# Kernel tuning notes

Measured on AMD Instinct MI355X. Metric: run time of the kernel, lower is better.

Reference implementation:

```python
import jax, jax.numpy as jnp
import numpy as np

N = 30000; E = 480000; B = 60
IN = 200; ID = 128; H = 128
NEXP = 4; TOPK = 2; TEMP = 1.5
HEADS = 4; DH = H // HEADS


def _ln(x, g, b):
    mu = jnp.mean(x, -1, keepdims=True)
    var = jnp.var(x, -1, keepdims=True)
    return (x - mu) / jnp.sqrt(var + 1e-5) * g + b


def _seg_sum(d, i, n):
    return jax.ops.segment_sum(d, i, num_segments=n)


def setup_inputs():
    key = jax.random.key(0)
    kit = iter(jax.random.split(key, 80))
    def w(*s):
        return jax.random.normal(next(kit), s, jnp.float32) * 0.05
    inp = {}
    inp['x'] = jax.random.normal(next(kit), (N, IN), jnp.float32)
    inp['node_identity'] = jax.random.normal(next(kit), (N, ID), jnp.float32)
    inp['edge_index'] = jax.random.randint(next(kit), (2, E), 0, N)
    inp['batch'] = jnp.sort(jax.random.randint(next(kit), (N,), 0, B))
    inp.update(fe_W=w(IN, H), fe_b=jnp.zeros(H), fe_g=jnp.ones(H), fe_be=jnp.zeros(H))
    inp.update(ie_W=w(ID, H), ie_b=jnp.zeros(H), ie_g=jnp.ones(H), ie_be=jnp.zeros(H))
    inp.update(fuse_W=w(2 * H, H), fuse_b=jnp.zeros(H), fuse_g=jnp.ones(H), fuse_be=jnp.zeros(H))
    inp.update(router_W=w(2 * H, NEXP))
    inp.update(mlp_W1=w(H, H), mlp_b1=jnp.zeros(H), mlp_W2=w(H, H), mlp_b2=jnp.zeros(H))
    inp.update(cheb_W=w(2, 2, H, H), cheb_b=jnp.zeros((2, H)))
    inp.update(gt_Wq=w(2, H, H), gt_bq=jnp.zeros((2, H)), gt_Wk=w(2, H, H), gt_bk=jnp.zeros((2, H)),
               gt_Wv=w(2, H, H), gt_bv=jnp.zeros((2, H)), gt_Ws=w(2, H, H), gt_bs=jnp.zeros((2, H)))
    inp.update(gcn_W=w(2, H, H), gcn_b=jnp.zeros((2, H)))
    inp.update(pn_g=jnp.ones((NEXP, H)), pn_b=jnp.zeros((NEXP, H)), expert_scales=jnp.ones(NEXP))
    inp.update(h1_W=w(H, H), h1_b=jnp.zeros(H), h1_g=jnp.ones(H), h1_be=jnp.zeros(H))
    inp.update(h2_W=w(H, H // 2), h2_b=jnp.zeros(H // 2), h2_g=jnp.ones(H // 2), h2_be=jnp.zeros(H // 2))
    inp.update(h3_W=w(H // 2, 2), h3_b=jnp.zeros(2), logit_bias=jnp.zeros(2))
    return inp


def _forward(x, node_identity, edge_index, batch, fe_W, fe_b, fe_g, fe_be, ie_W, ie_b, ie_g, ie_be,
             fuse_W, fuse_b, fuse_g, fuse_be, router_W, mlp_W1, mlp_b1, mlp_W2, mlp_b2, cheb_W, cheb_b,
             gt_Wq, gt_bq, gt_Wk, gt_bk, gt_Wv, gt_bv, gt_Ws, gt_bs, gcn_W, gcn_b, pn_g, pn_b,
             expert_scales, h1_W, h1_b, h1_g, h1_be, h2_W, h2_b, h2_g, h2_be, h3_W, h3_b, logit_bias):
    relu = jax.nn.relu
    src, dst = edge_index[0], edge_index[1]
    # encoders + fuse
    h_x = relu(_ln(x @ fe_W + fe_b, fe_g, fe_be))
    h_id = relu(_ln(node_identity @ ie_W + ie_b, ie_g, ie_be))
    h_router = jnp.concatenate([h_x, h_id], -1)
    h = relu(_ln(h_router @ fuse_W + fuse_b, fuse_g, fuse_be))
    # noisy top-k router (eval: no noise, no dropout)
    node_logits = h_router @ router_W
    probs = jax.nn.softmax(node_logits / TEMP, -1)
    vals, idx = jax.lax.top_k(probs, TOPK)
    wts = vals / jnp.clip(jnp.sum(vals, -1, keepdims=True), 1e-9)
    gates = jnp.zeros_like(probs).at[jnp.arange(N)[:, None], idx].set(wts)  # [N, 4]
    # degree / normalization terms
    ones_e = jnp.ones(E, jnp.float32)
    deg = _seg_sum(ones_e, dst, N)
    dinv = jnp.where(deg > 0, jax.lax.rsqrt(jnp.maximum(deg, 1.0)), 0.0)
    dinvl = jax.lax.rsqrt(deg + 1.0)  # with self loops (GCN)
    enorm = dinv[src] * dinv[dst]
    enorml = dinvl[src] * dinvl[dst]
    def aprop(xx, en, di_self=None):
        out = _seg_sum(xx[src] * en[:, None], dst, N)
        if di_self is not None:
            out = out + xx * di_self[:, None]
        return out
    # Expert 0: MLP (2 layers)
    e0 = relu(h @ mlp_W1 + mlp_b1) @ mlp_W2 + mlp_b2
    # Expert 1: ChebNet K=2 (lambda_max=2 -> L_hat = -A_norm), 2 layers
    z = h
    for l in range(2):
        tx1 = -aprop(z, enorm)
        z = z @ cheb_W[l, 0] + tx1 @ cheb_W[l, 1] + cheb_b[l]
        if l == 0:
            z = relu(z)
    e1 = z
    # Expert 2: Graph Transformer, 2 layers, heads=4, root-weight skip
    z = h
    for l in range(2):
        q = (z @ gt_Wq[l] + gt_bq[l]).reshape(N, HEADS, DH)
        k = (z @ gt_Wk[l] + gt_bk[l]).reshape(N, HEADS, DH)
        v = (z @ gt_Wv[l] + gt_bv[l]).reshape(N, HEADS, DH)
        logits = jnp.sum(q[dst] * k[src], -1) * (1.0 / DH ** 0.5)  # [E, heads]
        m = jax.ops.segment_max(logits, dst, num_segments=N)
        m = jnp.where(jnp.isfinite(m), m, 0.0)
        p = jnp.exp(logits - m[dst])
        denom = jnp.clip(_seg_sum(p, dst, N), 1e-9)
        attn = p / denom[dst]
        agg = _seg_sum(attn[:, :, None] * v[src], dst, N).reshape(N, H)
        z = agg + z @ gt_Ws[l] + gt_bs[l]
        if l == 0:
            z = relu(z)
    e2 = z
    # Expert 3: GCN, 2 layers, self loops
    z = h
    for l in range(2):
        zw = z @ gcn_W[l]
        z = aprop(zw, enorml, dinvl * dinvl) + gcn_b[l]
        if l == 0:
            z = relu(z)
    e3 = z
    # per-expert post-norm, scale, gated combine + residual
    eo = jnp.stack([e0, e1, e2, e3], 0)  # [4, N, H]
    eo = _ln(eo, pn_g[:, None, :], pn_b[:, None, :]) * expert_scales[:, None, None]
    out = h + jnp.einsum('ne,enh->nh', gates, eo)
    # mean-pool readout per graph
    counts = jnp.clip(_seg_sum(jnp.ones(N, jnp.float32), batch, B), 1.0)
    pooled = _seg_sum(out, batch, B) / counts[:, None]
    # classification head
    zc = relu(_ln(pooled @ h1_W + h1_b, h1_g, h1_be))
    zc = relu(_ln(zc @ h2_W + h2_b, h2_g, h2_be))
    return zc @ h3_W + h3_b + logit_bias


def reference(x, node_identity, edge_index, batch, fe_W, fe_b, fe_g, fe_be, ie_W, ie_b, ie_g, ie_be,
              fuse_W, fuse_b, fuse_g, fuse_be, router_W, mlp_W1, mlp_b1, mlp_W2, mlp_b2, cheb_W, cheb_b,
              gt_Wq, gt_bq, gt_Wk, gt_bk, gt_Wv, gt_bv, gt_Ws, gt_bs, gcn_W, gcn_b, pn_g, pn_b,
              expert_scales, h1_W, h1_b, h1_g, h1_be, h2_W, h2_b, h2_g, h2_be, h3_W, h3_b, logit_bias):
    return _forward(x, node_identity, edge_index, batch, fe_W, fe_b, fe_g, fe_be, ie_W, ie_b, ie_g, ie_be,
                    fuse_W, fuse_b, fuse_g, fuse_be, router_W, mlp_W1, mlp_b1, mlp_W2, mlp_b2, cheb_W, cheb_b,
                    gt_Wq, gt_bq, gt_Wk, gt_bk, gt_Wv, gt_bv, gt_Ws, gt_bs, gcn_W, gcn_b, pn_g, pn_b,
                    expert_scales, h1_W, h1_b, h1_g, h1_be, h2_W, h2_b, h2_g, h2_be, h3_W, h3_b, logit_bias)
```

## Files before the change

kernel.cpp:

```cpp
#include <hip/hip_runtime.h>

#define PCH   32
#define NWT   19
#define SCH   2048

typedef unsigned short ushort_t;
typedef __attribute__((ext_vector_type(8))) short bf16x8;
typedef __attribute__((ext_vector_type(4))) float f32x4;

__device__ __forceinline__ float bf2f(unsigned int v) {
    return __uint_as_float(v << 16);
}
__device__ __forceinline__ unsigned int f2bu(float f) {
    unsigned int u = __float_as_uint(f);
    return (u + 0x7fffu + ((u >> 16) & 1u)) >> 16;
}
__device__ __forceinline__ void unpack8(uint4 u, float* f) {
    f[0] = bf2f(u.x & 0xffff); f[1] = bf2f(u.x >> 16);
    f[2] = bf2f(u.y & 0xffff); f[3] = bf2f(u.y >> 16);
    f[4] = bf2f(u.z & 0xffff); f[5] = bf2f(u.z >> 16);
    f[6] = bf2f(u.w & 0xffff); f[7] = bf2f(u.w >> 16);
}
__device__ __forceinline__ uint4 pack8(const float* f) {
    uint4 p;
// ... 596 lines not shown
            *(uint4*)&Bs[rows[j]][kofs[j] + 8] = bvb[j][1];
        }
        __syncthreads();
#pragma unroll
        for (int t = 16; t < 32; t++) {
            bf16x8 bf = *(const bf16x8*)&Bs[(t - 16) * 16 + l16][q * 8];
            acc[t] = __builtin_amdgcn_mfma_f32_16x16x32_bf16(af, bf, acc[t], 0, 0, 0);
        }
    }
    const float* bs4[4] = {b0, b1, b2, b3};
#pragma unroll
    for (int s = 0; s < 4; s++) {
#pragma unroll
        for (int t8 = 0; t8 < 8; t8++) {
            int t = s * 8 + t8;
            int col = t8 * 16 + l16;
            float bb = bs4[s][col];
#pragma unroll
            for (int r = 0; r < 4; r++) {
                int row = m0 + 16 * wv + q * 4 + r;
                float val = acc[t][r] + bb;
                float other = __shfl_xor(val, 1);
                if (!(lane & 1) && row < M) {
                    unsigned int pk = f2bu(val) | (f2bu(other) << 16);
                    if (s == 0)
                        *(unsigned int*)(qb + (size_t)row * 128 + col) = pk;
                    else if (s == 3)
                        *(unsigned int*)(sk + (size_t)row * 128 + col) = pk;
                    else
                        *(unsigned int*)(kv + (size_t)row * 256 + (s - 1) * 128 + col) = pk;
                }
            }
        }
    }
}

__device__ __forceinline__ void gemm_wv_dev(const ushort_t* __restrict__ A,
                                            const ushort_t* __restrict__ Wt,
                                            ushort_t* __restrict__ Cb, int M,
                                            const float* __restrict__ bias, int relu,
                                            int w, int lane)
{
    const int K = 128;
    int ct = w & 3;
    int rt = w >> 2;
    int row0 = rt * 16;
    if (row0 >= M) return;
    int l16 = lane & 15, q = lane >> 4;
    int arow = row0 + l16;
    bool aok = arow < M;
    const ushort_t* Ar = A + (size_t)arow * K + q * 8;
    const ushort_t* W0 = Wt + (size_t)(ct * 32 + l16) * K + q * 8;
    const ushort_t* W1 = W0 + (size_t)16 * K;
    bf16x8 zz = {0, 0, 0, 0, 0, 0, 0, 0};
    f32x4 a0 = {0.f, 0.f, 0.f, 0.f}, a1 = {0.f, 0.f, 0.f, 0.f};
#pragma unroll
    for (int k0 = 0; k0 < K; k0 += 32) {
        bf16x8 af = aok ? *(const bf16x8*)(Ar + k0) : zz;
        bf16x8 b0 = *(const bf16x8*)(W0 + k0);
        bf16x8 b1 = *(const bf16x8*)(W1 + k0);
        a0 = __builtin_amdgcn_mfma_f32_16x16x32_bf16(af, b0, a0, 0, 0, 0);
        a1 = __builtin_amdgcn_mfma_f32_16x16x32_bf16(af, b1, a1, 0, 0, 0);
    }
    f32x4 av[2] = {a0, a1};
#pragma unroll
    for (int t = 0; t < 2; t++) {
        int col = ct * 32 + t * 16 + l16;
        float bb = bias ? bias[col] : 0.f;
#pragma unroll
        for (int r = 0; r < 4; r++) {
            int row = row0 + q * 4 + r;
            float val = av[t][r] + bb;
            if (relu) val = fmaxf(val, 0.f);
            float other = __shfl_xor(val, 1);
            if (!(l16 & 1) && row < M) {
                unsigned int pk = f2bu(val) | (f2bu(other) << 16);
                *(unsigned int*)(Cb + (size_t)row * 128 + col) = pk;
            }
        }
    }
}

__device__ __forceinline__ void gather2_dev(const ushort_t* __restrict__ Xb,
                                            ushort_t* __restrict__ OutA, ushort_t* __restrict__ OutB,
                                            const int* __restrict__ rowptr, const int* __restrict__ csr,
                                            const float* __restrict__ ecA, const float* __restrict__ ecB,
                                            const float* __restrict__ dinvl, int M, int bx)
{
    int node = bx * 4 + (threadIdx.x >> 6);
    int lane = threadIdx.x & 63;
    if (node >= M) return;
    int beg = rowptr[node], end = rowptr[node + 1];
    int slot = lane >> 4, g = lane & 15;
    float aA[8] = {0, 0, 0, 0, 0, 0, 0, 0};
    float aB[8] = {0, 0, 0, 0, 0, 0, 0, 0};

    float cAa = 0.f, cBa = 0.f, cAb = 0.f, cBb = 0.f;
    int na = 0, nb = 0;
    float nAa = 0.f, nBa = 0.f, nAb = 0.f, nBb = 0.f;
    uint4 xA, xB;
    {
        int r0 = beg + slot, r1 = beg + 4 + slot;
        int ia = 0, ib = 0;
        if (r0 < end) { ia = csr[r0]; cAa = ecA[r0]; cBa = ecB[r0]; }
        if (r1 < end) { ib = csr[r1]; cAb = ecA[r1]; cBb = ecB[r1]; }
        xA = *(const uint4*)(Xb + (size_t)ia * 128 + g * 8);
        xB = *(const uint4*)(Xb + (size_t)ib * 128 + g * 8);
    }
    {
        int r0 = beg + 8 + slot, r1 = beg + 12 + slot;
        if (r0 < end) { na = csr[r0]; nAa = ecA[r0]; nBa = ecB[r0]; }
        if (r1 < end) { nb = csr[r1]; nAb = ecA[r1]; nBb = ecB[r1]; }
    }
    for (int e = beg; e < end; e += 8) {
        uint4 xA2 = *(const uint4*)(Xb + (size_t)na * 128 + g * 8);
        uint4 xB2 = *(const uint4*)(Xb + (size_t)nb * 128 + g * 8);
        int r0 = e + 16 + slot, r1 = e + 20 + slot;
        int ma = 0, mb = 0;
        float mAa = 0.f, mBa = 0.f, mAb = 0.f, mBb = 0.f;
        if (r0 < end) { ma = csr[r0]; mAa = ecA[r0]; mBa = ecB[r0]; }
        if (r1 < end) { mb = csr[r1]; mAb = ecA[r1]; mBb = ecB[r1]; }
        fma8(xA, cAa, aA); fma8(xA, cBa, aB);
        fma8(xB, cAb, aA); fma8(xB, cBb, aB);
        xA = xA2; xB = xB2;
        cAa = nAa; cBa = nBa; cAb = nAb; cBb = nBb;
        na = ma; nb = mb;
        nAa = mAa; nBa = mBa; nAb = mAb; nBb = mBb;
    }
#pragma unroll
    for (int j = 0; j < 8; j++) {
        aA[j] += __shfl_xor(aA[j], 16); aA[j] += __shfl_xor(aA[j], 32);
        aB[j] += __shfl_xor(aB[j], 16); aB[j] += __shfl_xor(aB[j], 32);
    }
    {
        float c = dinvl[node]; c *= c;
        uint4 xs = *(const uint4*)(Xb + (size_t)node * 128 + g * 8);
        fma8(xs, c, aB);
    }
    if (lane < 16) {
        float oA[8], oB[8];
#pragma unroll
        for (int j = 0; j < 8; j++) { oA[j] = -aA[j]; oB[j] = aB[j]; }
        size_t ofs = (size_t)node * 128 + g * 8;
        *(uint4*)(OutA + ofs) = pack8(oA);
        *(uint4*)(OutB + ofs) = pack8(oB);
    }
}

__device__ __forceinline__ void gather_l2_dev(const ushort_t* __restrict__ XA,
                                              const ushort_t* __restrict__ XB,
                                              ushort_t* __restrict__ OutA, ushort_t* __restrict__ OutB,
                                              const int* __restrict__ rowptr, const int* __restrict__ csr,
                                              const float* __restrict__ ecA, const float* __restrict__ ecB,
                                              const float* __restrict__ dinvl, int M, int bx)
{
    int node = bx * 4 + (threadIdx.x >> 6);
    int lane = threadIdx.x & 63;
    if (node >= M) return;
    int beg = rowptr[node], end = rowptr[node + 1];
    int slot = lane >> 4, g = lane & 15;
    float aA[8] = {0, 0, 0, 0, 0, 0, 0, 0};
    float aB[8] = {0, 0, 0, 0, 0, 0, 0, 0};

    float cAa = 0.f, cBa = 0.f, cAb = 0.f, cBb = 0.f;
    int na = 0, nb = 0;
    float nAa = 0.f, nBa = 0.f, nAb = 0.f, nBb = 0.f;
    uint4 ra, rb, sa, sb;
    {
        int r0 = beg + slot, r1 = beg + 4 + slot;
        int ia = 0, ib = 0;
        if (r0 < end) { ia = csr[r0]; cAa = ecA[r0]; cBa = ecB[r0]; }
        if (r1 < end) { ib = csr[r1]; cAb = ecA[r1]; cBb = ecB[r1]; }
        ra = *(const uint4*)(XA + (size_t)ia * 128 + g * 8);
        rb = *(const uint4*)(XA + (size_t)ib * 128 + g * 8);
        sa = *(const uint4*)(XB + (size_t)ia * 128 + g * 8);
        sb = *(const uint4*)(XB + (size_t)ib * 128 + g * 8);
    }
    {
        int r0 = beg + 8 + slot, r1 = beg + 12 + slot;
        if (r0 < end) { na = csr[r0]; nAa = ecA[r0]; nBa = ecB[r0]; }
        if (r1 < end) { nb = csr[r1]; nAb = ecA[r1]; nBb = ecB[r1]; }
    }
    for (int e = beg; e < end; e += 8) {
        uint4 ra2 = *(const uint4*)(XA + (size_t)na * 128 + g * 8);
        uint4 rb2 = *(const uint4*)(XA + (size_t)nb * 128 + g * 8);
        uint4 sa2 = *(const uint4*)(XB + (size_t)na * 128 + g * 8);
        uint4 sb2 = *(const uint4*)(XB + (size_t)nb * 128 + g * 8);
        int r0 = e + 16 + slot, r1 = e + 20 + slot;
        int ma = 0, mb = 0;
        float mAa = 0.f, mBa = 0.f, mAb = 0.f, mBb = 0.f;
        if (r0 < end) { ma = csr[r0]; mAa = ecA[r0]; mBa = ecB[r0]; }
        if (r1 < end) { mb = csr[r1]; mAb = ecA[r1]; mBb = ecB[r1]; }
        fma8(ra, cAa, aA); fma8(rb, cAb, aA);
        fma8(sa, cBa, aB); fma8(sb, cBb, aB);
        ra = ra2; rb = rb2; sa = sa2; sb = sb2;
        cAa = nAa; cBa = nBa; cAb = nAb; cBb = nBb;
        na = ma; nb = mb;
        nAa = mAa; nBa = mBa; nAb = mAb; nBb = mBb;
    }
#pragma unroll
    for (int j = 0; j < 8; j++) {
        aA[j] += __shfl_xor(aA[j], 16); aA[j] += __shfl_xor(aA[j], 32);
        aB[j] += __shfl_xor(aB[j], 16); aB[j] += __shfl_xor(aB[j], 32);
    }
    {
        float c = dinvl[node]; c *= c;
        uint4 xs = *(const uint4*)(XB + (size_t)node * 128 + g * 8);
        fma8(xs, c, aB);
    }
    if (lane < 16) {
        float oA[8], oB[8];
#pragma unroll
        for (int j = 0; j < 8; j++) { oA[j] = -aA[j]; oB[j] = aB[j]; }
        size_t ofs = (size_t)node * 128 + g * 8;
        *(uint4*)(OutA + ofs) = pack8(oA);
        *(uint4*)(OutB + ofs) = pack8(oB);
    }
}

__device__ __forceinline__ void gt_attn_dev(const ushort_t* __restrict__ Qb,
                                            const ushort_t* __restrict__ KV,
                                            const int* __restrict__ rowptr, const int* __restrict__ csr,
                                            const ushort_t* __restrict__ sk, int relu,
                                            ushort_t* __restrict__ Outb, int M, int bx)
{
    const float SCL = 0.17677669529663689f * 1.4426950408889634f;
    int node = bx * 4 + (threadIdx.x >> 6);
    int lane = threadIdx.x & 63;
    if (node >= M) return;
    int beg = rowptr[node], end = rowptr[node + 1];
    int slot = lane >> 4, g = lane & 15;
    uint4 qv = *(const uint4*)(Qb + (size_t)node * 128 + g * 8);
    float qf[8];
    unpack8(qv, qf);
#pragma unroll
    for (int j = 0; j < 8; j++) qf[j] *= SCL;
    float ax[8] = {0, 0, 0, 0, 0, 0, 0, 0};
    float den = 0.f;

    bool va = false, vb = false;
    int na = 0, nb = 0;
    bool wa = false, wb = false;
    uint4 kA, kB, uA, uB;
    {
        int r0 = beg + slot, r1 = beg + 4 + slot;
        va = r0 < end; vb = r1 < end;
        int ia = va ? csr[r0] : 0;
        int ib = vb ? csr[r1] : 0;
        const ushort_t* p0 = KV + (size_t)ia * 256 + g * 8;
        const ushort_t* p1 = KV + (size_t)ib * 256 + g * 8;
        kA = *(const uint4*)p0; uA = *(const uint4*)(p0 + 128);
        kB = *(const uint4*)p1; uB = *(const uint4*)(p1 + 128);
    }
    {
        int r0 = beg + 8 + slot, r1 = beg + 12 + slot;
        wa = r0 < end; wb = r1 < end;
        na = wa ? csr[r0] : 0;
        nb = wb ? csr[r1] : 0;
    }
    for (int e = beg; e < end; e += 8) {
        const ushort_t* p0 = KV + (size_t)na * 256 + g * 8;
        const ushort_t* p1 = KV + (size_t)nb * 256 + g * 8;
        uint4 kA2 = *(const uint4*)p0;
        uint4 uA2 = *(const uint4*)(p0 + 128);
        uint4 kB2 = *(const uint4*)p1;
        uint4 uB2 = *(const uint4*)(p1 + 128);
        int r0 = e + 16 + slot, r1 = e + 20 + slot;
        bool xa = r0 < end, xb = r1 < end;
        int ma = xa ? csr[r0] : 0;
        int mb = xb ? csr[r1] : 0;
        float d0 = dot8(kA, qf);
        float d1 = dot8(kB, qf);
        d0 += __shfl_xor(d0, 1); d0 += __shfl_xor(d0, 2);
        d1 += __shfl_xor(d1, 1); d1 += __shfl_xor(d1, 2);
        float w0 = va ? exp2f(fminf(d0, 80.f)) : 0.f;
        float w1 = vb ? exp2f(fminf(d1, 80.f)) : 0.f;
        den += w0 + w1;
        fma8(uA, w0, ax);
        fma8(uB, w1, ax);
        kA = kA2; kB = kB2; uA = uA2; uB = uB2;
        va = wa; vb = wb;
        wa = xa; wb = xb; na = ma; nb = mb;
    }
#pragma unroll
    for (int j = 0; j < 8; j++) {
        ax[j] += __shfl_xor(ax[j], 16); ax[j] += __shfl_xor(ax[j], 32);
    }
    den += __shfl_xor(den, 16); den += __shfl_xor(den, 32);
    float dd = fmaxf(den, 1e-9f);
    if (lane < 16) {
        uint4 sv = *(const uint4*)(sk + (size_t)node * 128 + g * 8);
        float sf[8];
        unpack8(sv, sf);
        float o[8];
#pragma unroll
        for (int j = 0; j < 8; j++) {
            float v = ax[j] / dd + sf[j];
            o[j] = relu ? fmaxf(v, 0.f) : v;
        }
        *(uint4*)(Outb + (size_t)node * 128 + g * 8) = pack8(o);
    }
}

__global__ void flatA_kernel(const ushort_t* __restrict__ hb,
                             ushort_t* __restrict__ x1, ushort_t* __restrict__ x2,
                             const int* __restrict__ rowptr, const int* __restrict__ csr,
                             const float* __restrict__ ecA, const float* __restrict__ ecB,
                             const float* __restrict__ dinvl, int N,
                             const ushort_t* __restrict__ wmlp1, ushort_t* __restrict__ xm,
                             const float* __restrict__ b18)
{
    int bx = blockIdx.x;
    int gN4 = (N + 3) >> 2;
    if (bx < gN4) {
        gather2_dev(hb, x1, x2, rowptr, csr, ecA, ecB, dinvl, N, bx);
    } else {
        int w = (bx - gN4) * 4 + (threadIdx.x >> 6);
        gemm_wv_dev(hb, wmlp1, xm, N, b18, 1, w, threadIdx.x & 63);
    }
}

__global__ __launch_bounds__(256)
void megaA_kernel(const ushort_t* __restrict__ hb,
                  const ushort_t* __restrict__ wqkvs,
                  ushort_t* __restrict__ qb, ushort_t* __restrict__ kvb, ushort_t* __restrict__ skb,
                  const float* __restrict__ bq, const float* __restrict__ bk,
                  const float* __restrict__ bv, const float* __restrict__ bs,
                  const ushort_t* __restrict__ x1, const ushort_t* __restrict__ wch0,
                  const ushort_t* __restrict__ wch1, ushort_t* __restrict__ x0,
                  const float* __restrict__ bch,
                  const ushort_t* __restrict__ x2, const ushort_t* __restrict__ wgcn,
                  ushort_t* __restrict__ xg1, const float* __restrict__ bgcn,
                  int M)
{
    __shared__ ushort_t As[64][40];
    __shared__ ushort_t Bs[256][40];
    int y = blockIdx.y, bx = blockIdx.x;
    if (y == 0) gemm4_dev(As, Bs, hb, wqkvs, qb, kvb, skb, M, bq, bk, bv, bs, bx);
    else if (y == 1) gemm_dual_dev(As, Bs, hb, wch0, x1, wch1, x0, M, bch, 1, bx);
    else gemm_bf_dev<128>(As, Bs, x2, wgcn, xg1, M, bgcn, 1, bx);
}

__global__ void flatB_kernel(const ushort_t* __restrict__ qb, const ushort_t* __restrict__ kvb,
                             const int* __restrict__ rowptr, const int* __restrict__ csr,
                             const ushort_t* __restrict__ skb, ushort_t* __restrict__ aout,
                             const ushort_t* __restrict__ x0, const ushort_t* __restrict__ xg1,
                             ushort_t* __restrict__ x3, ushort_t* __restrict__ x2,
                             const float* __restrict__ ecA, const float* __restrict__ ecB,
                             const float* __restrict__ dinvl, int N)
{
    int bx = blockIdx.x;
    int gN4 = (N + 3) >> 2;
    if (bx < gN4) gt_attn_dev(qb, kvb, rowptr, csr, skb, 1, aout, N, bx);
    else gather_l2_dev(x0, xg1, x3, x2, rowptr, csr, ecA, ecB, dinvl, N, bx - gN4);
}

__global__ __launch_bounds__(256)
void megaB_kernel(const ushort_t* __restrict__ x1,
                  const ushort_t* __restrict__ wqkvs,
                  ushort_t* __restrict__ qb, ushort_t* __restrict__ kvb, ushort_t* __restrict__ skb,
                  const float* __restrict__ bq, const float* __restrict__ bk,
                  const float* __restrict__ bv, const float* __restrict__ bs,
                  const ushort_t* __restrict__ x0, const ushort_t* __restrict__ wch0,
                  const ushort_t* __restrict__ x3, const ushort_t* __restrict__ wch1,
                  ushort_t* __restrict__ e1b, const float* __restrict__ bch,
                  const ushort_t* __restrict__ x2, const ushort_t* __restrict__ wgcn,
                  ushort_t* __restrict__ e3b, const float* __restrict__ bgcn,
                  const ushort_t* __restrict__ xm, const ushort_t* __restrict__ wmlp2,
                  ushort_t* __restrict__ e0b, const float* __restrict__ bmlp2,
                  int M)
{
    __shared__ ushort_t As[64][40];
    __shared__ ushort_t Bs[256][40];
    int y = blockIdx.y, bx = blockIdx.x;
    if (y == 0) gemm4_dev(As, Bs, x1, wqkvs, qb, kvb, skb, M, bq, bk, bv, bs, bx);
    else if (y == 1) gemm_dual_dev(As, Bs, x0, wch0, x3, wch1, e1b, M, bch, 0, bx);
    else if (y == 2) gemm_bf_dev<128>(As, Bs, x2, wgcn, e3b, M, bgcn, 0, bx);
    else gemm_bf_dev<128>(As, Bs, xm, wmlp2, e0b, M, bmlp2, 0, bx);
}

__global__ void gt_attn2_kernel(const ushort_t* __restrict__ Qb, const ushort_t* __restrict__ KV,
                                const int* __restrict__ rowptr, const int* __restrict__ csr,
                                const ushort_t* __restrict__ sk,
                                ushort_t* __restrict__ Outb, int M)
{
    gt_attn_dev(Qb, KV, rowptr, csr, sk, 0, Outb, M, blockIdx.x);
}

__global__ void pool_combine_kernel(const ushort_t* __restrict__ hb,
                                    const ushort_t* __restrict__ e0, const ushort_t* __restrict__ e1,
                                    const ushort_t* __restrict__ e2, const ushort_t* __restrict__ e3,
                                    const float* __restrict__ gates,
                                    const float* __restrict__ png, const float* __restrict__ pnb,
                                    const float* __restrict__ esc,
                                    const int* __restrict__ bstart, const int* __restrict__ bend,
                                    float* __restrict__ partial)
{
    int b = blockIdx.x, c = blockIdx.y;
    int lane = threadIdx.x;
    int s0 = bstart[b], e0i = bend[b];
    const ushort_t* eps[4] = {e0, e1, e2, e3};
    float ga[4], gb[4], ba[4], bb[4], es[4];
#pragma unroll
    for (int ee = 0; ee < 4; ee++) {
        ga[ee] = png[ee * 128 + lane * 2];
        gb[ee] = png[ee * 128 + lane * 2 + 1];
        ba[ee] = pnb[ee * 128 + lane * 2];
        bb[ee] = pnb[ee * 128 + lane * 2 + 1];
        es[ee] = esc[ee];
    }
    float sx = 0.f, sy = 0.f;
    for (int n = s0 + c; n < e0i; n += PCH) {
        size_t ofs = (size_t)n * 128 + lane * 2;
        float4 gg = *(const float4*)(gates + (size_t)n * 4);
        float gv[4] = {gg.x, gg.y, gg.z, gg.w};
        unsigned int hu = *(const unsigned int*)(hb + ofs);
        float ox = bf2f(hu & 0xffff), oy = bf2f(hu >> 16);
#pragma unroll
        for (int ee = 0; ee < 4; ee++) {
            unsigned int u = *(const unsigned int*)(eps[ee] + ofs);
            float vx = bf2f(u & 0xffff), vy = bf2f(u >> 16);
            float su = vx + vy, sq = vx * vx + vy * vy;
#pragma unroll
            for (int off = 32; off; off >>= 1) { su += __shfl_xor(su, off); sq += __shfl_xor(sq, off); }
            float mean = su * (1.f / 128.f);
            float var = sq * (1.f / 128.f) - mean * mean;
            float inv = rsqrtf(var + 1e-5f);
            float cc = es[ee] * gv[ee];
            ox = fmaf(cc, (vx - mean) * inv * ga[ee] + ba[ee], ox);
            oy = fmaf(cc, (vy - mean) * inv * gb[ee] + bb[ee], oy);
        }
        sx += ox; sy += oy;
    }
    *(float2*)(partial + ((size_t)b * PCH + c) * 128 + lane * 2) = make_float2(sx, sy);
}

__global__ void head_kernel(const float* __restrict__ partial,
                            const int* __restrict__ bstart, const int* __restrict__ bend,
                            const float* __restrict__ h1W, const float* __restrict__ h1b,
                            const float* __restrict__ h1g, const float* __restrict__ h1be,
                            const float* __restrict__ h2W, const float* __restrict__ h2b,
                            const float* __restrict__ h2g, const float* __restrict__ h2be,
                            const float* __restrict__ h3W, const float* __restrict__ h3b,
                            const float* __restrict__ lbias,
                            float* __restrict__ out, int B)
{
    __shared__ float p[128], z[128];
    int b = blockIdx.x, t = threadIdx.x;
    float sum = 0.f;
#pragma unroll
    for (int c = 0; c < PCH; c++) sum += partial[((size_t)b * PCH + c) * 128 + t];
    float cnt = fmaxf((float)(bend[b] - bstart[b]), 1.f);
    p[t] = sum / cnt;
    __syncthreads();
    float a = h1b[t];
    for (int k = 0; k < 128; k++) a = fmaf(p[k], h1W[k * 128 + t], a);
    z[t] = a;
    __syncthreads();
    float s = 0.f, sq = 0.f;
    for (int k = 0; k < 128; k++) { float x = z[k]; s += x; sq += x * x; }
    float mean = s * (1.f / 128.f), var = sq * (1.f / 128.f) - mean * mean;
    float y = fmaxf((a - mean) * rsqrtf(var + 1e-5f) * h1g[t] + h1be[t], 0.f);
    __syncthreads();
    z[t] = y;
    __syncthreads();
    float a2 = 0.f;
    if (t < 64) {
        a2 = h2b[t];
        for (int k = 0; k < 128; k++) a2 = fmaf(z[k], h2W[k * 64 + t], a2);
    }
    __syncthreads();
    if (t < 64) p[t] = a2;
    __syncthreads();
    if (t < 2) {
        float s2 = 0.f, sq2 = 0.f;
        for (int k = 0; k < 64; k++) { float x = p[k]; s2 += x; sq2 += x * x; }
        float mean2 = s2 * (1.f / 64.f), var2 = sq2 * (1.f / 64.f) - mean2 * mean2;
        float inv2 = rsqrtf(var2 + 1e-5f);
        float o = h3b[t] + lbias[t];
        for (int k = 0; k < 64; k++) {
            float zc = fmaxf((p[k] - mean2) * inv2 * h2g[k] + h2be[k], 0.f);
            o = fmaf(zc, h3W[k * 2 + t], o);
        }
        out[b * 2 + t] = o;
    }
}

extern "C" void kernel_launch(void* const* d_in, const int* in_sizes, int n_in,
                              void* d_out, int out_size, void* d_ws, size_t ws_size,
                              hipStream_t stream)
{
    (void)ws_size; (void)n_in;
    const int N = in_sizes[3];
    const int E = in_sizes[2] / 2;
    const int B = out_size / 2;

    const int* ei = (const int*)d_in[2];
    const int* src = ei;
    const int* dst = ei + E;
    const int* batch = (const int*)d_in[3];

    const float* W[47];
    for (int i = 0; i < 47; i++) W[i] = (const float*)d_in[i];

    size_t fN = (size_t)N;
    float* gates   = (float*)d_ws;
    float* dinv    = gates + 4 * fN;
    float* dinvl   = dinv + fN;
    float* partial = dinvl + fN;
    float* logitsA = partial + (size_t)128 * B * PCH;
    float* logitsB = logitsA + 4 * fN;
    ushort_t* hb  = (ushort_t*)(logitsB + 4 * fN);
    ushort_t* e0b = hb + 128 * fN;
    ushort_t* e1b = e0b + 128 * fN;
    ushort_t* e2b = e1b + 128 * fN;
    ushort_t* e3b = e2b + 128 * fN;
    ushort_t* x0  = e3b + 128 * fN;
    ushort_t* x1  = x0 + 128 * fN;
    ushort_t* x2  = x1 + 128 * fN;
    ushort_t* x3  = x2 + 128 * fN;
    ushort_t* xm  = x3 + 128 * fN;
    ushort_t* xg1 = xm + 128 * fN;
    ushort_t* skb = xg1 + 128 * fN;
    ushort_t* qb  = skb + 128 * fN;
    ushort_t* kvb = qb + 128 * fN;
    ushort_t* hrb = kvb + 256 * fN;
    ushort_t* wt  = hrb + 256 * fN;
    WtPack wp;
    const float* wsrc[NWT] = {
        W[4], W[8], W[12], W[17], W[19],
        W[21], W[21] + 16384, W[21] + 32768, W[21] + 49152,
        W[23], W[25], W[27], W[29],
        W[23] + 16384, W[25] + 16384, W[27] + 16384, W[29] + 16384,
        W[31], W[31] + 16384
    };
    const int wk[NWT] = {200, 128, 256, 128, 128,
                         128, 128, 128, 128,
                         128, 128, 128, 128,
                         128, 128, 128, 128,
                         128, 128};
    unsigned long long woff[NWT];
    unsigned long long acc_off = 0;
    for (int i = 0; i < NWT; i++) {
        wp.src[i] = wsrc[i];
        wp.K[i] = wk[i];
        wp.off[i] = acc_off;
        woff[i] = acc_off;
        acc_off += (unsigned long long)128 * wk[i];
    }
    int* degi   = (int*)(wt + acc_off + 8);
    int* cursor = degi + N;
    int* rowptr = cursor + N;
    int* csr    = rowptr + (N + 1);
    int* bstart = csr + E;
    int* bend   = bstart + B;
    int* bsum   = bend + B;
    float* ecA  = (float*)(bsum + 256);
    float* ecB  = ecA + E;

    dim3 blk(256);
    int gN4 = (N + 3) / 4;
    int gG = (N + 63) / 64;
    int RT = (N + 15) / 16;
    int nsb = (N + SCH - 1) / SCH;
    int nseg = (N + 255) / 256;
    int nedge = (E + 255) / 256;

    hipMemsetAsync(degi, 0, (size_t)2 * N * sizeof(int), stream);
    hipMemsetAsync(bstart, 0, (size_t)2 * B * sizeof(int), stream);

    setup_mega_kernel<<<dim3(608 + nseg + nedge), blk, 0, stream>>>(
        wp, wt, batch, bstart, bend, N, dst, degi, E);
    scan1_kernel<<<dim3(nsb), blk, 0, stream>>>(degi, rowptr, bsum, N);
    scan2_kernel<<<1, blk, 0, stream>>>(bsum, nsb);
    EncCfg c0 = {W[0], 200, 200, wt + woff[0], hrb, W[5], W[6], W[7], W[16], logitsA};
    EncCfg c1 = {W[1], 128, 128, wt + woff[1], hrb + 128, W[9], W[10], W[11], W[16] + 512, logitsB};
    scan3_enc_kernel<<<dim3(nseg + 2 * gG), blk, 0, stream>>>(
        rowptr, bsum, degi, dinv, dinvl, N, c0, c1);
    ln_csr_topk_kernel<<<dim3(gG + nedge + nseg), blk, 0, stream>>>(
        hrb, wt + woff[2], hb, N, W[13], W[14], W[15],
        src, dst, rowptr, cursor, csr, dinv, dinvl, ecA, ecB, E,
        logitsA, logitsB, gates);
    flatA_kernel<<<dim3(gN4 + RT), blk, 0, stream>>>(hb, x1, x2, rowptr, csr, ecA, ecB,
                                                     dinvl, N, wt + woff[3], xm, W[18]);
    megaA_kernel<<<dim3(gG, 3), blk, 0, stream>>>(
        hb, wt + woff[9], qb, kvb, skb, W[24], W[26], W[28], W[30],
        x1, wt + woff[5], wt + woff[6], x0, W[22],
        x2, wt + woff[17], xg1, W[32], N);
    flatB_kernel<<<dim3(2 * gN4), blk, 0, stream>>>(
        qb, kvb, rowptr, csr, skb, x1,
        x0, xg1, x3, x2, ecA, ecB, dinvl, N);
    megaB_kernel<<<dim3(gG, 4), blk, 0, stream>>>(
        x1, wt + woff[13], qb, kvb, skb,
        W[24] + 128, W[26] + 128, W[28] + 128, W[30] + 128,
        x0, wt + woff[7], x3, wt + woff[8], e1b, W[22] + 128,
        x2, wt + woff[18], e3b, W[32] + 128,
        xm, wt + woff[4], e0b, W[20], N);
    gt_attn2_kernel<<<dim3(gN4), blk, 0, stream>>>(qb, kvb, rowptr, csr, skb, e2b, N);
    pool_combine_kernel<<<dim3(B, PCH), dim3(64), 0, stream>>>(
        hb, e0b, e1b, e2b, e3b, gates, W[33], W[34], W[35], bstart, bend, partial);
    head_kernel<<<dim3(B), dim3(128), 0, stream>>>(partial, bstart, bend,
        W[36], W[37], W[38], W[39],
        W[40], W[41], W[42], W[43],
        W[44], W[45], W[46],
        (float*)d_out, B);
}
```

Baseline: 546.6 us.

## Regroup expert stages into four launches mixing gathers, attention and GEMMs

Reorders the dependency schedule of the four expert branches. The five launches (flatA, megaA, flatB, megaB, gt_attn2) become four fused stage kernels. Each stage mixes independent memory-bound gather/attention blocks with compute-bound GEMM blocks, and the MLP second layer moves to the wavefront GEMV path. A separate buffer xa1 holds the first attention output so it no longer overwrites x1, and the Chebyshev/GCN stages use a smaller 128-row B tile in shared memory. The aim is to remove one launch and its barrier and to overlap heterogeneous work. The cost is that heterogeneous blocks in one grid compete for occupancy and may be unevenly balanced.

```diff
diff --git a/kernel.cpp b/kernel.cpp
--- a/kernel.cpp
+++ b/kernel.cpp
@@ -922,89 +922,102 @@
     }
 }
 
-__global__ void flatA_kernel(const ushort_t* __restrict__ hb,
-                             ushort_t* __restrict__ x1, ushort_t* __restrict__ x2,
-                             const int* __restrict__ rowptr, const int* __restrict__ csr,
-                             const float* __restrict__ ecA, const float* __restrict__ ecB,
-                             const float* __restrict__ dinvl, int N,
-                             const ushort_t* __restrict__ wmlp1, ushort_t* __restrict__ xm,
-                             const float* __restrict__ b18)
-{
+__global__ __launch_bounds__(256)
+void stage1_kernel(const ushort_t* __restrict__ hb,
+                   ushort_t* __restrict__ x1, ushort_t* __restrict__ x2,
+                   const int* __restrict__ rowptr, const int* __restrict__ csr,
+                   const float* __restrict__ ecA, const float* __restrict__ ecB,
+                   const float* __restrict__ dinvl, int N,
+                   const ushort_t* __restrict__ wmlp1, ushort_t* __restrict__ xm,
+                   const float* __restrict__ bmlp1,
+                   const ushort_t* __restrict__ wqkvs,
+                   ushort_t* __restrict__ qb, ushort_t* __restrict__ kvb,
+                   ushort_t* __restrict__ skb,
+                   const float* __restrict__ bq, const float* __restrict__ bk,
+                   const float* __restrict__ bv, const float* __restrict__ bs)
+{
+    __shared__ ushort_t As[64][40];
+    __shared__ ushort_t Bs[256][40];
     int bx = blockIdx.x;
     int gN4 = (N + 3) >> 2;
+    int RT = (N + 15) >> 4;
     if (bx < gN4) {
         gather2_dev(hb, x1, x2, rowptr, csr, ecA, ecB, dinvl, N, bx);
+    } else if (bx < gN4 + RT) {
+        int w = (bx - gN4) * 4 + (threadIdx.x >> 6);
+        gemm_wv_dev(hb, wmlp1, xm, N, bmlp1, 1, w, threadIdx.x & 63);
     } else {
-        int w = (bx - gN4) * 4 + (threadIdx.x >> 6);
-        gemm_wv_dev(hb, wmlp1, xm, N, b18, 1, w, threadIdx.x & 63);
+        gemm4_dev(As, Bs, hb, wqkvs, qb, kvb, skb, N, bq, bk, bv, bs, bx - gN4 - RT);
     }
 }
 
 __global__ __launch_bounds__(256)
-void megaA_kernel(const ushort_t* __restrict__ hb,
-                  const ushort_t* __restrict__ wqkvs,
-                  ushort_t* __restrict__ qb, ushort_t* __restrict__ kvb, ushort_t* __restrict__ skb,
-                  const float* __restrict__ bq, const float* __restrict__ bk,
-                  const float* __restrict__ bv, const float* __restrict__ bs,
-                  const ushort_t* __restrict__ x1, const ushort_t* __restrict__ wch0,
-                  const ushort_t* __restrict__ wch1, ushort_t* __restrict__ x0,
-                  const float* __restrict__ bch,
-                  const ushort_t* __restrict__ x2, const ushort_t* __restrict__ wgcn,
-                  ushort_t* __restrict__ xg1, const float* __restrict__ bgcn,
-                  int M)
+void stage2_kernel(const ushort_t* __restrict__ qb, const ushort_t* __restrict__ kvb,
+                   const int* __restrict__ rowptr, const int* __restrict__ csr,
+                   const ushort_t* __restrict__ skb, ushort_t* __restrict__ xa1,
+                   const ushort_t* __restrict__ hb, const ushort_t* __restrict__ wch0,
+                   const ushort_t* __restrict__ x1, const ushort_t* __restrict__ wch1,
+                   ushort_t* __restrict__ x0, const float* __restrict__ bch,
+                   const ushort_t* __restrict__ x2, const ushort_t* __restrict__ wgcn,
+                   ushort_t* __restrict__ xg1, const float* __restrict__ bgcn, int N)
+{
+    __shared__ ushort_t As[64][40];
+    __shared__ ushort_t Bs[128][40];
+    int bx = blockIdx.x;
+    int gN4 = (N + 3) >> 2;
+    int gG = (N + 63) >> 6;
+    if (bx < gN4) gt_attn_dev(qb, kvb, rowptr, csr, skb, 1, xa1, N, bx);
+    else if (bx < gN4 + gG) gemm_dual_dev(As, Bs, hb, wch0, x1, wch1, x0, N, bch, 1, bx - gN4);
+    else gemm_bf_dev<128>(As, Bs, x2, wgcn, xg1, N, bgcn, 1, bx - gN4 - gG);
+}
+
+__global__ __launch_bounds__(256)
+void stage3_kernel(const ushort_t* __restrict__ x0, const ushort_t* __restrict__ xg1,
+                   ushort_t* __restrict__ x3, ushort_t* __restrict__ x2,
+                   const int* __restrict__ rowptr, const int* __restrict__ csr,
+                   const float* __restrict__ ecA, const float* __restrict__ ecB,
+                   const float* __restrict__ dinvl, int N,
+                   const ushort_t* __restrict__ xm, const ushort_t* __restrict__ wmlp2,
+                   ushort_t* __restrict__ e0b, const float* __restrict__ bmlp2,
+                   const ushort_t* __restrict__ xa1, const ushort_t* __restrict__ wqkvs,
+                   ushort_t* __restrict__ qb, ushort_t* __restrict__ kvb,
+                   ushort_t* __restrict__ skb,
+                   const float* __restrict__ bq, const float* __restrict__ bk,
+                   const float* __restrict__ bv, const float* __restrict__ bs)
 {
     __shared__ ushort_t As[64][40];
     __shared__ ushort_t Bs[256][40];
-    int y = blockIdx.y, bx = blockIdx.x;
-    if (y == 0) gemm4_dev(As, Bs, hb, wqkvs, qb, kvb, skb, M, bq, bk, bv, bs, bx);
-    else if (y == 1) gemm_dual_dev(As, Bs, hb, wch0, x1, wch1, x0, M, bch, 1, bx);
-    else gemm_bf_dev<128>(As, Bs, x2, wgcn, xg1, M, bgcn, 1, bx);
-}
-
-__global__ void flatB_kernel(const ushort_t* __restrict__ qb, const ushort_t* __restrict__ kvb,
-                             const int* __restrict__ rowptr, const int* __restrict__ csr,
-                             const ushort_t* __restrict__ skb, ushort_t* __restrict__ aout,
-                             const ushort_t* __restrict__ x0, const ushort_t* __restrict__ xg1,
-                             ushort_t* __restrict__ x3, ushort_t* __restrict__ x2,
-                             const float* __restrict__ ecA, const float* __restrict__ ecB,
-                             const float* __restrict__ dinvl, int N)
-{
     int bx = blockIdx.x;
     int gN4 = (N + 3) >> 2;
-    if (bx < gN4) gt_attn_dev(qb, kvb, rowptr, csr, skb, 1, aout, N, bx);
-    else gather_l2_dev(x0, xg1, x3, x2, rowptr, csr, ecA, ecB, dinvl, N, bx - gN4);
+    int RT = (N + 15) >> 4;
+    if (bx < gN4) {
+        gather_l2_dev(x0, xg1, x3, x2, rowptr, csr, ecA, ecB, dinvl, N, bx);
+    } else if (bx < gN4 + RT) {
+        int w = (bx - gN4) * 4 + (threadIdx.x >> 6);
+        gemm_wv_dev(xm, wmlp2, e0b, N, bmlp2, 0, w, threadIdx.x & 63);
+    } else {
+        gemm4_dev(As, Bs, xa1, wqkvs, qb, kvb, skb, N, bq, bk, bv, bs, bx - gN4 - RT);
+    }
 }
 
 __global__ __launch_bounds__(256)
-void megaB_kernel(const ushort_t* __restrict__ x1,
-                  const ushort_t* __restrict__ wqkvs,
-                  ushort_t* __restrict__ qb, ushort_t* __restrict__ kvb, ushort_t* __restrict__ skb,
-                  const float* __restrict__ bq, const float* __restrict__ bk,
-                  const float* __restrict__ bv, const float* __restrict__ bs,
-                  const ushort_t* __restrict__ x0, const ushort_t* __restrict__ wch0,
-                  const ushort_t* __restrict__ x3, const ushort_t* __restrict__ wch1,
-                  ushort_t* __restrict__ e1b, const float* __restrict__ bch,
-                  const ushort_t* __restrict__ x2, const ushort_t* __restrict__ wgcn,
-                  ushort_t* __restrict__ e3b, const float* __restrict__ bgcn,
-                  const ushort_t* __restrict__ xm, const ushort_t* __restrict__ wmlp2,
-                  ushort_t* __restrict__ e0b, const float* __restrict__ bmlp2,
-                  int M)
+void stage4_kernel(const ushort_t* __restrict__ qb, const ushort_t* __restrict__ kvb,
+                   const int* __restrict__ rowptr, const int* __restrict__ csr,
+                   const ushort_t* __restrict__ skb, ushort_t* __restrict__ e2b,
+                   const ushort_t* __restrict__ x0, const ushort_t* __restrict__ wch0,
+                   const ushort_t* __restrict__ x3, const ushort_t* __restrict__ wch1,
+                   ushort_t* __restrict__ e1b, const float* __restrict__ bch,
+                   const ushort_t* __restrict__ x2, const ushort_t* __restrict__ wgcn,
+                   ushort_t* __restrict__ e3b, const float* __restrict__ bgcn, int N)
 {
     __shared__ ushort_t As[64][40];
-    __shared__ ushort_t Bs[256][40];
-    int y = blockIdx.y, bx = blockIdx.x;
-    if (y == 0) gemm4_dev(As, Bs, x1, wqkvs, qb, kvb, skb, M, bq, bk, bv, bs, bx);
-    else if (y == 1) gemm_dual_dev(As, Bs, x0, wch0, x3, wch1, e1b, M, bch, 0, bx);
-    else if (y == 2) gemm_bf_dev<128>(As, Bs, x2, wgcn, e3b, M, bgcn, 0, bx);
-    else gemm_bf_dev<128>(As, Bs, xm, wmlp2, e0b, M, bmlp2, 0, bx);
-}
-
-__global__ void gt_attn2_kernel(const ushort_t* __restrict__ Qb, const ushort_t* __restrict__ KV,
-                                const int* __restrict__ rowptr, const int* __restrict__ csr,
-                                const ushort_t* __restrict__ sk,
-                                ushort_t* __restrict__ Outb, int M)
-{
-    gt_attn_dev(Qb, KV, rowptr, csr, sk, 0, Outb, M, blockIdx.x);
+    __shared__ ushort_t Bs[128][40];
+    int bx = blockIdx.x;
+    int gN4 = (N + 3) >> 2;
+    int gG = (N + 63) >> 6;
+    if (bx < gN4) gt_attn_dev(qb, kvb, rowptr, csr, skb, 0, e2b, N, bx);
+    else if (bx < gN4 + gG) gemm_dual_dev(As, Bs, x0, wch0, x3, wch1, e1b, N, bch, 0, bx - gN4);
+    else gemm_bf_dev<128>(As, Bs, x2, wgcn, e3b, N, bgcn, 0, bx - gN4 - gG);
 }
 
 __global__ void pool_combine_kernel(const ushort_t* __restrict__ hb,
@@ -1142,7 +1155,8 @@
     ushort_t* xm  = x3 + 128 * fN;
     ushort_t* xg1 = xm + 128 * fN;
     ushort_t* skb = xg1 + 128 * fN;
-    ushort_t* qb  = skb + 128 * fN;
+    ushort_t* xa1 = skb + 128 * fN;
+    ushort_t* qb  = xa1 + 128 * fN;
     ushort_t* kvb = qb + 128 * fN;
     ushort_t* hrb = kvb + 256 * fN;
     ushort_t* wt  = hrb + 256 * fN;
@@ -1201,22 +1215,23 @@
         hrb, wt + woff[2], hb, N, W[13], W[14], W[15],
         src, dst, rowptr, cursor, csr, dinv, dinvl, ecA, ecB, E,
         logitsA, logitsB, gates);
-    flatA_kernel<<<dim3(gN4 + RT), blk, 0, stream>>>(hb, x1, x2, rowptr, csr, ecA, ecB,
-                                                     dinvl, N, wt + woff[3], xm, W[18]);
-    megaA_kernel<<<dim3(gG, 3), blk, 0, stream>>>(
-        hb, wt + woff[9], qb, kvb, skb, W[24], W[26], W[28], W[30],
-        x1, wt + woff[5], wt + woff[6], x0, W[22],
+    stage1_kernel<<<dim3(gN4 + RT + gG), blk, 0, stream>>>(
+        hb, x1, x2, rowptr, csr, ecA, ecB, dinvl, N,
+        wt + woff[3], xm, W[18],
+        wt + woff[9], qb, kvb, skb, W[24], W[26], W[28], W[30]);
+    stage2_kernel<<<dim3(gN4 + 2 * gG), blk, 0, stream>>>(
+        qb, kvb, rowptr, csr, skb, xa1,
+        hb, wt + woff[5], x1, wt + woff[6], x0, W[22],
         x2, wt + woff[17], xg1, W[32], N);
-    flatB_kernel<<<dim3(2 * gN4), blk, 0, stream>>>(
-        qb, kvb, rowptr, csr, skb, x1,
-        x0, xg1, x3, x2, ecA, ecB, dinvl, N);
-    megaB_kernel<<<dim3(gG, 4), blk, 0, stream>>>(
-        x1, wt + woff[13], qb, kvb, skb,
-        W[24] + 128, W[26] + 128, W[28] + 128, W[30] + 128,
+    stage3_kernel<<<dim3(gN4 + RT + gG), blk, 0, stream>>>(
+        x0, xg1, x3, x2, rowptr, csr, ecA, ecB, dinvl, N,
+        xm, wt + woff[4], e0b, W[20],
+        xa1, wt + woff[13], qb, kvb, skb,
+        W[24] + 128, W[26] + 128, W[28] + 128, W[30] + 128);
+    stage4_kernel<<<dim3(gN4 + 2 * gG), blk, 0, stream>>>(
+        qb, kvb, rowptr, csr, skb, e2b,
         x0, wt + woff[7], x3, wt + woff[8], e1b, W[22] + 128,
-        x2, wt + woff[18], e3b, W[32] + 128,
-        xm, wt + woff[4], e0b, W[20], N);
-    gt_attn2_kernel<<<dim3(gN4), blk, 0, stream>>>(qb, kvb, rowptr, csr, skb, e2b, N);
+        x2, wt + woff[18], e3b, W[32] + 128, N);
     pool_combine_kernel<<<dim3(B, PCH), dim3(64), 0, stream>>>(
         hb, e0b, e1b, e2b, e3b, gates, W[33], W[34], W[35], bstart, bend, partial);
     head_kernel<<<dim3(B), dim3(128), 0, stream>>>(partial, bstart, bend,
```

Result: slower. 678.5 us (+24.1%).
